# Kernel tuning notes

Measured on AMD Instinct MI355X. Metric: run time of the kernel, lower is better.

Reference implementation:

```python
import jax, jax.numpy as jnp
import numpy as np
from jax import lax

GAMMA = 1.0  # init gamma


def setup_inputs() -> dict:
    key = jax.random.key(0)
    k = jax.random.split(key, 6)
    B, T1, T2, D, WD = 64, 320, 320, 768, 32
    x = jax.random.normal(k[0], (B, T1, D), jnp.float32)
    y = jax.random.normal(k[1], (B, T2, D), jnp.float32)
    # nn.Linear(input_dim, warp_dim): weight [WD, D], bias [WD]
    W = jax.random.normal(k[2], (WD, D), jnp.float32) / np.sqrt(D).astype(np.float32)
    b = 0.01 * jax.random.normal(k[3], (WD,), jnp.float32)
    warp_scale = 1.0 + 0.1 * jax.random.normal(k[4], (WD,), jnp.float32)
    warp_shift = 0.1 * jax.random.normal(k[5], (WD,), jnp.float32)
    return {"x": x, "y": y, "W": W, "b": b, "warp_scale": warp_scale, "warp_shift": warp_shift}


def _soft_dtw_path(xw, yw, gamma):
    # Faithful banded soft-DTW DP: cells outside the band stay 0 and ARE read
    # by in-band neighbors, exactly as the torch loop does.
    B, T1, _ = xw.shape
    T2 = yw.shape[1]
    bw = max(T1, T2) // 4 + 1
    # squared euclidean distances [B,T1,T2] (expanded form to avoid B*T1*T2*D blow-up)
    x2 = jnp.sum(xw * xw, -1)[:, :, None]
    y2 = jnp.sum(yw * yw, -1)[:, None, :]
    dist = x2 + y2 - 2.0 * jnp.einsum('bid,bjd->bij', xw, yw)
    NEG = jnp.float32(-1e30)  # disables a candidate inside logsumexp
    t2s = jnp.arange(T2)

    def outer(prev_row, xs):  # prev_row: path[t1-1, :] of shape [B,T2]
        t1, drow = xs  # drow: dist[:, t1, :] -> [B,T2]
        diag_prev = jnp.concatenate([jnp.zeros((B, 1), drow.dtype), prev_row[:, :-1]], axis=1)

        def inner(left, ins):  # left: path[t1, t2-1] -> [B]
            t2, d, up, diag = ins
            z = jnp.stack([
                jnp.where((t1 > 0) & (t2 > 0), -diag / gamma, NEG),
                jnp.where(t1 > 0, -up / gamma, NEG),
                jnp.where(t2 > 0, -left / gamma, NEG),
            ], axis=0)  # [3,B]
            softmin = -gamma * jax.nn.logsumexp(z, axis=0)
            val = d + jnp.where((t1 > 0) | (t2 > 0), softmin, 0.0)
            in_band = (t2 >= t1 - bw) & (t2 <= t1 + bw - 1)
            val = jnp.where(in_band, val, 0.0)
            return val, val

        _, row = lax.scan(inner, jnp.zeros((B,), drow.dtype),
                          (t2s, drow.T, prev_row.T, diag_prev.T))
        row = row.T  # [B,T2]
        return row, row

    _, path = lax.scan(outer, jnp.zeros((B, T2), dist.dtype),
                       (jnp.arange(T1), jnp.transpose(dist, (1, 0, 2))))
    path = jnp.transpose(path, (1, 0, 2))  # [B,T1,T2]
    return jax.nn.softmax(-path / gamma, axis=-1)


def reference(x, y, W, b, warp_scale, warp_shift):
    xw = (x @ W.T + b) * warp_scale + warp_shift
    yw = (y @ W.T + b) * warp_scale + warp_shift
    path = _soft_dtw_path(xw, yw, GAMMA)  # [B,T1,T2] softmax probs
    pn = path / (jnp.sum(path, axis=1, keepdims=True) + 1e-10)
    aligned = jnp.einsum('bts,btd->bsd', pn, x)  # bmm(path^T, x) -> [B,T2,D]
    return aligned, path
```

## Files before the change

kernel.cpp:

```cpp
#include <hip/hip_runtime.h>

#define NB 64
#define T 320
#define D 768
#define WD 32
#define NSTEP 639
#define NBLK 80
#define BSTRIDE (NBLK * 1024)
#define BIG 1e30f
#define LOG2E 1.44269504088896340736f
#define LN2 0.69314718055994530942f

__device__ __forceinline__ float dpp_ror1(float v) {
  return __int_as_float(__builtin_amdgcn_update_dpp(
      0, __float_as_int(v), 0x13C, 0xF, 0xF, true));
}
__device__ __forceinline__ float dpp_rol1(float v) {
  return __int_as_float(__builtin_amdgcn_update_dpp(
      0, __float_as_int(v), 0x134, 0xF, 0xF, true));
}

__global__ __launch_bounds__(256) void prep_kernel(
    const float* __restrict__ W, const float* __restrict__ bias,
    const float* __restrict__ wscale, const float* __restrict__ wshift,
    float* __restrict__ WeT, float* __restrict__ beff) {
  int i = blockIdx.x * 256 + threadIdx.x;
  int c = i >> 5, k = i & 31;
  WeT[i] = W[k * D + c] * wscale[k];
  if (i < WD) beff[i] = bias[i] * wscale[i] + wshift[i];
}

__global__ __launch_bounds__(256) void proj_kernel(
    const float* __restrict__ x, const float* __restrict__ y,
    const float* __restrict__ WeT, const float* __restrict__ beff,
    float* __restrict__ xw, float* __restrict__ yw) {
  __shared__ float lds[8448];
  int tid = threadIdx.x;
  int w = tid >> 6, l = tid & 63;
  int rbase = blockIdx.x * 64;
  float acc[32];
#pragma unroll
  for (int k = 0; k < 32; ++k) acc[k] = 0.f;
#pragma clang loop unroll(disable)
  for (int ch = 0; ch < 6; ++ch) {
    __syncthreads();
#pragma unroll
    for (int p = 0; p < 8; ++p) {
      int idx = p * 256 + tid;
      int row = idx >> 5;
      int c4 = idx & 31;
      int r = rbase + row;
      const float* src = (r < NB * T) ? x + (size_t)r * D
                                      : y + (size_t)(r - NB * T) * D;
      float4 v = *(const float4*)(src + ch * 128 + c4 * 4);
      lds[row * 129 + c4 * 4 + 0] = v.x;
      lds[row * 129 + c4 * 4 + 1] = v.y;
      lds[row * 129 + c4 * 4 + 2] = v.z;
      lds[row * 129 + c4 * 4 + 3] = v.w;
    }
    __syncthreads();
    int woff = __builtin_amdgcn_readfirstlane((ch * 128 + w * 32) * 32);
    const float* wp = WeT + woff;
#pragma unroll
    for (int cc = 0; cc < 32; ++cc) {
      float xv = lds[l * 129 + w * 32 + cc];
#pragma unroll
      for (int k = 0; k < 32; ++k)
        acc[k] = fmaf(wp[cc * 32 + k], xv, acc[k]);
    }
  }
  __syncthreads();
#pragma unroll
  for (int k = 0; k < 32; ++k) lds[w * 2112 + l * 33 + k] = acc[k];
  __syncthreads();
  int idx = tid * 8;
  int row = idx >> 5;
  int k0 = idx & 31;
  float o[8];
#pragma unroll
  for (int e = 0; e < 8; ++e)
    o[e] = lds[0 * 2112 + row * 33 + k0 + e] + lds[1 * 2112 + row * 33 + k0 + e] +
           lds[2 * 2112 + row * 33 + k0 + e] + lds[3 * 2112 + row * 33 + k0 + e] +
           beff[k0 + e];
  int rr = rbase + row;
  float* dst = (rr < NB * T) ? xw + (size_t)rr * WD + k0
                             : yw + (size_t)(rr - NB * T) * WD + k0;
  float4 o0 = {o[0], o[1], o[2], o[3]}, o1 = {o[4], o[5], o[6], o[7]};
  *(float4*)dst = o0;
  *(float4*)(dst + 4) = o1;
}

__global__ __launch_bounds__(256) void dist_kernel(
    const float* __restrict__ xw, const float* __restrict__ yw,
    float* __restrict__ dc) {
  int b = blockIdx.y;
  int i = blockIdx.x * 256 + threadIdx.x;
  int dblk = i >> 10;
  int a = (i >> 3) & 127;
  int k = i & 7;
  if (a >= 81) return;
  int d = dblk * 8 + k;
  if (d >= NSTEP) return;
  int par = (d + 1) & 1;
  int base = (d + 81 - par) >> 1;
  int t1 = base - a;
  int t2 = d - t1;
  if ((unsigned)t1 >= (unsigned)T || (unsigned)t2 >= (unsigned)T) return;
  const float4* xr = (const float4*)(xw + ((size_t)b * T + t1) * WD);
  const float4* yr = (const float4*)(yw + ((size_t)b * T + t2) * WD);
  float s = 0.f;
#pragma unroll
  for (int q = 0; q < 8; ++q) {
    float4 xv = xr[q], yv = yr[q];
    float d0 = xv.x - yv.x, d1 = xv.y - yv.y, d2 = xv.z - yv.z, d3 = xv.w - yv.w;
    s = fmaf(d0, d0, s); s = fmaf(d1, d1, s); s = fmaf(d2, d2, s); s = fmaf(d3, d3, s);
  }
  dc[(size_t)b * BSTRIDE + i] = s * LOG2E;
}

#define FSTEP(DP_, DS_, PAR, DVAL)                                             \
  {                                                                            \
    const int d_ = (DVAL);                                                     \
    const int base_ = (d_ + 81 - (PAR)) >> 1;                                  \
    float shP, shS;                                                            \
    if (PAR) { shP = dpp_rol1((l == 0) ? v0b : v0); shS = dpp_rol1(v0b); }     \
    else     { shP = dpp_ror1(v1); shS = dpp_ror1((l == 63) ? v1 : v1b); }     \
    int t1 = base_ - l, t2 = d_ - t1;                                          \
    {                                                                          \
      bool valid = ((unsigned)t1 < (unsigned)T) && ((unsigned)t2 < (unsigned)T); \
      float up, left, diag;                                                    \
      if (PAR) { left = v0; up = shP; diag = v1; }                             \
      else     { up = v1; left = (l == 0) ? 0.f : shP; diag = v0; }            \
      float cu = (t1 > 0) ? up : BIG;                                          \
      float cl = (t2 > 0) ? left : BIG;                                        \
      float cd = (t1 > 0 && t2 > 0) ? diag : BIG;                              \
      float mn = fminf(fminf(cu, cl), cd);                                     \
      float mx = fmaxf(fmaxf(cu, cl), cd);                                     \
      float md = fmaxf(fminf(cu, cl), fminf(fmaxf(cu, cl), cd));               \
      float ss = 1.f + __builtin_amdgcn_exp2f(mn - md) +                       \
                 __builtin_amdgcn_exp2f(mn - mx);                              \
      float val = (DP_) + mn - __builtin_amdgcn_logf(ss);                      \
      if ((DVAL) == 0) val = (DP_);                                            \
      if (valid) {                                                             \
        if (PAR) v1 = val; else v0 = val;                                      \
        outb[t1 * T + t2] = val * LN2;                                         \
      }                                                                        \
    }                                                                          \
    {                                                                          \
      int t1b = t1 - 64, t2b = t2 + 64;                                        \
      bool valid = (l < 17) && ((unsigned)t1b < (unsigned)T) &&                \
                   ((unsigned)t2b < (unsigned)T);                              \
      float up, left, diag;                                                    \
      if (PAR) { left = v0b; up = (l == 16) ? 0.f : shS; diag = v1b; }         \
      else     { up = v1b; left = shS; diag = v0b; }                           \
      float cu = (t1b > 0) ? up : BIG;                                         \
      float cl = (t2b > 0) ? left : BIG;                                       \
      float cd = (t1b > 0 && t2b > 0) ? diag : BIG;                            \
      float mn = fminf(fminf(cu, cl), cd);                                     \
      float mx = fmaxf(fmaxf(cu, cl), cd);                                     \
      float md = fmaxf(fminf(cu, cl), fminf(fmaxf(cu, cl), cd));               \
      float ss = 1.f + __builtin_amdgcn_exp2f(mn - md) +                       \
                 __builtin_amdgcn_exp2f(mn - mx);                              \
      float val = (DS_) + mn - __builtin_amdgcn_logf(ss);                      \
      if (valid) {                                                             \
        if (PAR) v1b = val; else v0b = val;                                    \
        outb[t1b * T + t2b] = val * LN2;                                       \
      }                                                                        \
    }                                                                          \
  }

#define SSTEP(DP_, DS_, PAR, IOFF)                                             \
  {                                                                            \
    float shP, shS;                                                            \
    if (PAR) { shP = dpp_rol1((l == 0) ? v0b : v0); shS = dpp_rol1(v0b); }     \
    else     { shP = dpp_ror1(v1); shS = dpp_ror1((l == 63) ? v1 : v1b); }     \
    {                                                                          \
      float up, left, diag;                                                    \
      if (PAR) { left = v0; up = shP; diag = v1; }                             \
      else     { up = v1; left = (l == 0) ? 0.f : shP; diag = v0; }            \
      float mn = fminf(fminf(up, left), diag);                                 \
      float mx = fmaxf(fmaxf(up, left), diag);                                 \
      float md = fmaxf(fminf(up, left), fminf(fmaxf(up, left), diag));         \
      float ss = 1.f + __builtin_amdgcn_exp2f(mn - md) +                       \
                 __builtin_amdgcn_exp2f(mn - mx);                              \
      float val = (DP_) + mn - __builtin_amdgcn_logf(ss);                      \
      if (PAR) v1 = val; else v0 = val;                                        \
      outb[io + (IOFF)] = val * LN2;                                           \
    }                                                                          \
    {                                                                          \
      float up, left, diag;                                                    \
      if (PAR) { left = v0b; up = (l == 16) ? 0.f : shS; diag = v1b; }         \
      else     { up = v1b; left = shS; diag = v0b; }                           \
      float mn = fminf(fminf(up, left), diag);                                 \
      float mx = fmaxf(fmaxf(up, left), diag);                                 \
      float md = fmaxf(fminf(up, left), fminf(fmaxf(up, left), diag));         \
      float ss = 1.f + __builtin_amdgcn_exp2f(mn - md) +                       \
                 __builtin_amdgcn_exp2f(mn - mx);                              \
      float val = (DS_) + mn - __builtin_amdgcn_logf(ss);                      \
      if (PAR) v1b = val; else v0b = val;                                      \
      if (l < 17) outb[ioS + (IOFF)] = val * LN2;                              \
    }                                                                          \
  }

#define LOADBLK(R0, R1, S0v, S1v, DBLK)                                        \
  {                                                                            \
    const float4* q_ = (const float4*)(dcb + (DBLK) * 1024 + l * 8);           \
    R0 = q_[0]; R1 = q_[1];                                                    \
    const float4* q2_ = (const float4*)(dcb + (DBLK) * 1024 + (64 + l) * 8);   \
    S0v = q2_[0]; S1v = q2_[1];                                                \
  }

#define BLK8_F(P0, P1, S0v, S1v, DB)                                           \
  FSTEP(P0.x, S0v.x, 1, (DB) + 0) FSTEP(P0.y, S0v.y, 0, (DB) + 1)              \
  FSTEP(P0.z, S0v.z, 1, (DB) + 2) FSTEP(P0.w, S0v.w, 0, (DB) + 3)              \
  FSTEP(P1.x, S1v.x, 1, (DB) + 4) FSTEP(P1.y, S1v.y, 0, (DB) + 5)              \
  FSTEP(P1.z, S1v.z, 1, (DB) + 6) FSTEP(P1.w, S1v.w, 0, (DB) + 7)

#define BLK8_S(P0, P1, S0v, S1v)                                               \
  SSTEP(P0.x, S0v.x, 1, 0)   SSTEP(P0.y, S0v.y, 0, 320)                        \
  SSTEP(P0.z, S0v.z, 1, 321) SSTEP(P0.w, S0v.w, 0, 641)                        \
  io += 642; ioS += 642;                                                       \
  SSTEP(P1.x, S1v.x, 1, 0)   SSTEP(P1.y, S1v.y, 0, 320)                        \
  SSTEP(P1.z, S1v.z, 1, 321) SSTEP(P1.w, S1v.w, 0, 641)                        \
  io += 642; ioS += 642;

__global__ __launch_bounds__(64) void dtw_kernel(
    const float* __restrict__ dc, float* __restrict__ path) {
  int b = blockIdx.x;
  int l = threadIdx.x;
  const float* dcb = dc + (size_t)b * BSTRIDE;
  float* outb = path + (size_t)b * T * T;
  float v0 = 0.f, v1 = 0.f, v0b = 0.f, v1b = 0.f;
  float4 aP0, aP1, aS0, aS1, bP0, bP1, bS0, bS1;
  int io = 0, ioS = 0;

  if (l == 40) {
    float d00 = dcb[320];
    v1 = d00;
    outb[0] = d00 * LN2;
  }
  LOADBLK(aP0, aP1, aS0, aS1, 0)
#pragma clang loop unroll(disable)
  for (int it = 0; it < 6; ++it) {
    int dbase = it * 16;
    int blk = it * 2;
    LOADBLK(bP0, bP1, bS0, bS1, blk + 1)
    BLK8_F(aP0, aP1, aS0, aS1, dbase)
    LOADBLK(aP0, aP1, aS0, aS1, blk + 2)
    BLK8_F(bP0, bP1, bS0, bS1, dbase + 8)
  }
  io = 28168 - 319 * l;
  ioS = io - 20416;
#pragma clang loop unroll(disable)
  for (int it = 0; it < 27; ++it) {
    int blk = 12 + it * 2;
    LOADBLK(bP0, bP1, bS0, bS1, blk + 1)
    BLK8_S(aP0, aP1, aS0, aS1)
    LOADBLK(aP0, aP1, aS0, aS1, blk + 2)
    BLK8_S(bP0, bP1, bS0, bS1)
  }
#pragma clang loop unroll(disable)
  for (int it = 0; it < 6; ++it) {
    int dbase = 528 + it * 16;
    int blk = 66 + it * 2;
    LOADBLK(bP0, bP1, bS0, bS1, blk + 1)
    BLK8_F(aP0, aP1, aS0, aS1, dbase)
    LOADBLK(aP0, aP1, aS0, aS1, blk + 2)
    BLK8_F(bP0, bP1, bS0, bS1, dbase + 8)
  }
  LOADBLK(bP0, bP1, bS0, bS1, 79)
  BLK8_F(aP0, aP1, aS0, aS1, 624)
  FSTEP(bP0.x, bS0.x, 1, 632) FSTEP(bP0.y, bS0.y, 0, 633)
  FSTEP(bP0.z, bS0.z, 1, 634) FSTEP(bP0.w, bS0.w, 0, 635)
  FSTEP(bP1.x, bS1.x, 1, 636) FSTEP(bP1.y, bS1.y, 0, 637)
  FSTEP(bP1.z, bS1.z, 1, 638)
}

__global__ __launch_bounds__(T) void softmax_kernel(float* __restrict__ path,
                                                    float* __restrict__ cvec) {
  __shared__ float sm1[5], sm2[5];
  int row = blockIdx.x;
  int t1 = row % T;
  int j = threadIdx.x;
  float* p = path + (size_t)row * T;
  bool in = (j >= t1 - 81) && (j <= t1 + 80);
  float v = in ? p[j] : 0.f;
  float m = v;
#pragma unroll
  for (int off = 32; off >= 1; off >>= 1) m = fminf(m, __shfl_xor(m, off, 64));
  int w = j >> 6;
  if ((j & 63) == 0) sm1[w] = m;
  __syncthreads();
  m = fminf(fminf(fminf(sm1[0], sm1[1]), fminf(sm1[2], sm1[3])), sm1[4]);
  float e = __expf(m - v);
  float s = e;
#pragma unroll
  for (int off = 32; off >= 1; off >>= 1) s += __shfl_xor(s, off, 64);
  if ((j & 63) == 0) sm2[w] = s;
  __syncthreads();
  s = sm2[0] + sm2[1] + sm2[2] + sm2[3] + sm2[4];
  p[j] = e / s;
  if (j == 0) cvec[row] = __expf(m - 0.f) / s;
}

__global__ __launch_bounds__(256) void gk_kernel(
    const float* __restrict__ x, const float* __restrict__ cvec,
    float* __restrict__ g) {
  int b = blockIdx.y;
  int d0 = blockIdx.x * 256 + threadIdx.x;
  const float* xb = x + (size_t)b * T * D + d0;
  const float* cb = cvec + b * T;
  float s = 0.f;
  for (int t = 0; t < T; ++t) s = fmaf(cb[t], xb[(size_t)t * D], s);
  g[b * D + d0] = s;
}

__global__ __launch_bounds__(T) void colsum_kernel(
    const float* __restrict__ path, float* __restrict__ scale) {
  int b = blockIdx.x;
  int j = threadIdx.x;
  const float* p = path + (size_t)b * T * T;
  float s = 0.f;
  for (int t = 0; t < T; ++t) s += p[(size_t)t * T + j];
  scale[b * T + j] = 1.f / (s + 1e-10f);
}

#define TSB 64
#define TDB 256
#define TKB 16
__global__ __launch_bounds__(256) void bmm_kernel(
    const float* __restrict__ path, const float* __restrict__ x,
    const float* __restrict__ cvec, const float* __restrict__ g,
    const float* __restrict__ scale, float* __restrict__ out) {
  __shared__ __align__(16) float Pl[TKB][TSB];
  __shared__ __align__(16) float Xl[TKB][TDB];
  int b = blockIdx.z;
  int s0 = blockIdx.y * TSB;
  int d0 = blockIdx.x * TDB;
  int tid = threadIdx.x;
  int ts = tid & 7, td = tid >> 3;
  const float* pb = path + (size_t)b * T * T;
  const float* xb = x + (size_t)b * T * D;
  const float* cb = cvec + b * T;
  float acc[8][8];
  {
    const float* gb = g + b * D + d0 + td * 8;
    float4 g0 = *(const float4*)gb;
    float4 g1 = *(const float4*)(gb + 4);
    float gv[8] = {g0.x, g0.y, g0.z, g0.w, g1.x, g1.y, g1.z, g1.w};
#pragma unroll
    for (int i = 0; i < 8; ++i)
#pragma unroll
      for (int jj = 0; jj < 8; ++jj) acc[i][jj] = gv[jj];
  }
  int t_lo = s0 - 80; if (t_lo < 0) t_lo = 0; t_lo &= ~15;
  int t_hi = (s0 + 160) & ~15; if (t_hi > T) t_hi = T;
  for (int t0 = t_lo; t0 < t_hi; t0 += TKB) {
    __syncthreads();
    {
      int tr = tid >> 4, sc = (tid & 15) * 4;
      float4 p4 = *(const float4*)&pb[(size_t)(t0 + tr) * T + s0 + sc];
      float cv = cb[t0 + tr];
      p4.x -= cv; p4.y -= cv; p4.z -= cv; p4.w -= cv;
      *(float4*)&Pl[tr][sc] = p4;
    }
    {
      int tr = tid >> 4, c0 = (tid & 15) * 4;
#pragma unroll
      for (int q = 0; q < 4; ++q)
        *(float4*)&Xl[tr][c0 + q * 64] =
            *(const float4*)&xb[(size_t)(t0 + tr) * D + d0 + c0 + q * 64];
    }
    __syncthreads();
#pragma unroll
    for (int t = 0; t < TKB; ++t) {
      float4 pa = *(const float4*)&Pl[t][ts * 8];
      float4 pc = *(const float4*)&Pl[t][ts * 8 + 4];
      float4 xa = *(const float4*)&Xl[t][td * 8];
      float4 xc = *(const float4*)&Xl[t][td * 8 + 4];
      float pv[8] = {pa.x, pa.y, pa.z, pa.w, pc.x, pc.y, pc.z, pc.w};
      float xv[8] = {xa.x, xa.y, xa.z, xa.w, xc.x, xc.y, xc.z, xc.w};
#pragma unroll
      for (int i = 0; i < 8; ++i)
#pragma unroll
        for (int jj = 0; jj < 8; ++jj)
          acc[i][jj] = fmaf(pv[i], xv[jj], acc[i][jj]);
    }
  }
#pragma unroll
  for (int i = 0; i < 8; ++i) {
    int s = s0 + ts * 8 + i;
    float sc = scale[b * T + s];
    float* op = out + ((size_t)b * T + s) * D + d0 + td * 8;
    float4 o0, o1;
    o0.x = acc[i][0] * sc; o0.y = acc[i][1] * sc; o0.z = acc[i][2] * sc; o0.w = acc[i][3] * sc;
    o1.x = acc[i][4] * sc; o1.y = acc[i][5] * sc; o1.z = acc[i][6] * sc; o1.w = acc[i][7] * sc;
    *(float4*)op = o0;
    *(float4*)(op + 4) = o1;
  }
}

extern "C" void kernel_launch(void* const* d_in, const int* in_sizes, int n_in,
                              void* d_out, int out_size, void* d_ws, size_t ws_size,
                              hipStream_t stream) {
  const float* x = (const float*)d_in[0];
  const float* y = (const float*)d_in[1];
  const float* W = (const float*)d_in[2];
  const float* bias = (const float*)d_in[3];
  const float* wscale = (const float*)d_in[4];
  const float* wshift = (const float*)d_in[5];
  float* outp = (float*)d_out;
  float* aligned = outp;
  float* path = outp + (size_t)NB * T * D;
  float* distc = aligned;
  float* ws = (float*)d_ws;
  float* xw = ws;
  float* yw = xw + (size_t)NB * T * WD;
  float* scale = yw + (size_t)NB * T * WD;
  float* WeT = scale + (size_t)NB * T;
  float* beff = WeT + (size_t)WD * D;
  float* cvec = beff + WD;
  float* g = cvec + (size_t)NB * T;

  prep_kernel<<<dim3((WD * D) / 256), 256, 0, stream>>>(W, bias, wscale, wshift, WeT, beff);
  proj_kernel<<<dim3((2 * NB * T) / 64), 256, 0, stream>>>(x, y, WeT, beff, xw, yw);
  dist_kernel<<<dim3(BSTRIDE / 256, NB), 256, 0, stream>>>(xw, yw, distc);
  dtw_kernel<<<dim3(NB), 64, 0, stream>>>(distc, path);
  softmax_kernel<<<dim3(NB * T), T, 0, stream>>>(path, cvec);
  gk_kernel<<<dim3(D / 256, NB), 256, 0, stream>>>(x, cvec, g);
  colsum_kernel<<<dim3(NB), T, 0, stream>>>(path, scale);
  bmm_kernel<<<dim3(D / TDB, T / TSB, NB), 256, 0, stream>>>(path, x, cvec, g, scale, aligned);
}
```

Before: 374.5 us.

## Double-buffer bmm tiles, remap blocks for XCD locality, band-limit colsum

The bmm kernel now prefetches the next path/x tile into registers while computing on the current shared-memory buffer, and writes it into a second buffer, so there is one barrier per chunk instead of two. A 1D grid is remapped so consecutive blocks spread across XCDs while related tiles share L2. The colsum kernel uses more blocks and reads only the band region of each column, adding back the per-row constant cvec for out-of-band entries. The band-limited colsum depends on softmax values outside the band equaling cvec, and double buffering doubles shared memory per block.

Result: slower. 410.7 us (+9.7%).

```diff
diff --git a/kernel.cpp b/kernel.cpp
--- a/kernel.cpp
+++ b/kernel.cpp
@@ -315,14 +315,36 @@
   g[b * D + d0] = s;
 }
 
-__global__ __launch_bounds__(T) void colsum_kernel(
-    const float* __restrict__ path, float* __restrict__ scale) {
-  int b = blockIdx.x;
-  int j = threadIdx.x;
-  const float* p = path + (size_t)b * T * T;
+__global__ __launch_bounds__(256) void colsum_kernel(
+    const float* __restrict__ path, const float* __restrict__ cvec,
+    float* __restrict__ scale) {
+  __shared__ float red[4][64];
+  __shared__ float cbred[4];
+  int b = blockIdx.y;
+  int tid = threadIdx.x;
+  int l = tid & 63, tq = tid >> 6;
+  int j = blockIdx.x * 64 + l;
+  const float* cb = cvec + b * T;
+  float c = cb[tid];
+  if (tid < 64) c += cb[256 + tid];
+#pragma unroll
+  for (int off = 32; off >= 1; off >>= 1) c += __shfl_xor(c, off, 64);
+  if (l == 0) cbred[tq] = c;
   float s = 0.f;
-  for (int t = 0; t < T; ++t) s += p[(size_t)t * T + j];
-  scale[b * T + j] = 1.f / (s + 1e-10f);
+  int t0 = j - 80 + tq * 41;
+  const float* p = path + (size_t)b * T * T + j;
+#pragma unroll 4
+  for (int i = 0; i < 41; ++i) {
+    int t = t0 + i;
+    if ((unsigned)t < (unsigned)T) s += p[(size_t)t * T] - cb[t];
+  }
+  red[tq][l] = s;
+  __syncthreads();
+  if (tq == 0) {
+    float cs = red[0][l] + red[1][l] + red[2][l] + red[3][l] +
+               (cbred[0] + cbred[1] + cbred[2] + cbred[3]);
+    scale[b * T + j] = 1.f / (cs + 1e-10f);
+  }
 }
 
 #define TSB 64
@@ -332,11 +354,14 @@
     const float* __restrict__ path, const float* __restrict__ x,
     const float* __restrict__ cvec, const float* __restrict__ g,
     const float* __restrict__ scale, float* __restrict__ out) {
-  __shared__ __align__(16) float Pl[TKB][TSB];
-  __shared__ __align__(16) float Xl[TKB][TDB];
-  int b = blockIdx.z;
-  int s0 = blockIdx.y * TSB;
-  int d0 = blockIdx.x * TDB;
+  __shared__ __align__(16) float Pl[2][TKB][TSB];
+  __shared__ __align__(16) float Xl[2][TKB][TDB];
+  int bid = blockIdx.x;
+  int wgid = (bid & 7) * 120 + (bid >> 3);
+  int b = wgid / 15;
+  int r = wgid - b * 15;
+  int s0 = (r / 3) * TSB;
+  int d0 = (r % 3) * TDB;
   int tid = threadIdx.x;
   int ts = tid & 7, td = tid >> 3;
   const float* pb = path + (size_t)b * T * T;
@@ -355,29 +380,44 @@
   }
   int t_lo = s0 - 80; if (t_lo < 0) t_lo = 0; t_lo &= ~15;
   int t_hi = (s0 + 160) & ~15; if (t_hi > T) t_hi = T;
-  for (int t0 = t_lo; t0 < t_hi; t0 += TKB) {
-    __syncthreads();
-    {
-      int tr = tid >> 4, sc = (tid & 15) * 4;
-      float4 p4 = *(const float4*)&pb[(size_t)(t0 + tr) * T + s0 + sc];
-      float cv = cb[t0 + tr];
-      p4.x -= cv; p4.y -= cv; p4.z -= cv; p4.w -= cv;
-      *(float4*)&Pl[tr][sc] = p4;
-    }
-    {
-      int tr = tid >> 4, c0 = (tid & 15) * 4;
-#pragma unroll
-      for (int q = 0; q < 4; ++q)
-        *(float4*)&Xl[tr][c0 + q * 64] =
-            *(const float4*)&xb[(size_t)(t0 + tr) * D + d0 + c0 + q * 64];
-    }
-    __syncthreads();
+  int nch = (t_hi - t_lo) >> 4;
+  int str = tid >> 4;
+  int psc = (tid & 15) * 4;
+  float4 pr, xr0, xr1, xr2, xr3;
+  float cvr;
+#define BMM_LOAD(T0)                                                        \
+  {                                                                         \
+    pr = *(const float4*)&pb[(size_t)((T0) + str) * T + s0 + psc];          \
+    cvr = cb[(T0) + str];                                                   \
+    const float* xrow = &xb[(size_t)((T0) + str) * D + d0 + psc];           \
+    xr0 = *(const float4*)(xrow);                                           \
+    xr1 = *(const float4*)(xrow + 64);                                      \
+    xr2 = *(const float4*)(xrow + 128);                                     \
+    xr3 = *(const float4*)(xrow + 192);                                     \
+  }
+#define BMM_WRITE(BUF)                                                      \
+  {                                                                         \
+    float4 pw = pr;                                                         \
+    pw.x -= cvr; pw.y -= cvr; pw.z -= cvr; pw.w -= cvr;                     \
+    *(float4*)&Pl[BUF][str][psc] = pw;                                      \
+    *(float4*)&Xl[BUF][str][psc] = xr0;                                     \
+    *(float4*)&Xl[BUF][str][psc + 64] = xr1;                                \
+    *(float4*)&Xl[BUF][str][psc + 128] = xr2;                               \
+    *(float4*)&Xl[BUF][str][psc + 192] = xr3;                               \
+  }
+  BMM_LOAD(t_lo)
+  BMM_WRITE(0)
+  __syncthreads();
+  int cur = 0;
+#pragma clang loop unroll(disable)
+  for (int ch = 0; ch < nch; ++ch) {
+    if (ch + 1 < nch) { BMM_LOAD(t_lo + (ch + 1) * TKB) }
 #pragma unroll
     for (int t = 0; t < TKB; ++t) {
-      float4 pa = *(const float4*)&Pl[t][ts * 8];
-      float4 pc = *(const float4*)&Pl[t][ts * 8 + 4];
-      float4 xa = *(const float4*)&Xl[t][td * 8];
-      float4 xc = *(const float4*)&Xl[t][td * 8 + 4];
+      float4 pa = *(const float4*)&Pl[cur][t][ts * 8];
+      float4 pc = *(const float4*)&Pl[cur][t][ts * 8 + 4];
+      float4 xa = *(const float4*)&Xl[cur][t][td * 8];
+      float4 xc = *(const float4*)&Xl[cur][t][td * 8 + 4];
       float pv[8] = {pa.x, pa.y, pa.z, pa.w, pc.x, pc.y, pc.z, pc.w};
       float xv[8] = {xa.x, xa.y, xa.z, xa.w, xc.x, xc.y, xc.z, xc.w};
 #pragma unroll
@@ -385,6 +425,11 @@
 #pragma unroll
         for (int jj = 0; jj < 8; ++jj)
           acc[i][jj] = fmaf(pv[i], xv[jj], acc[i][jj]);
+    }
+    if (ch + 1 < nch) {
+      BMM_WRITE(cur ^ 1)
+      __syncthreads();
+      cur ^= 1;
     }
   }
 #pragma unroll
@@ -428,6 +473,6 @@
   dtw_kernel<<<dim3(NB), 64, 0, stream>>>(distc, path);
   softmax_kernel<<<dim3(NB * T), T, 0, stream>>>(path, cvec);
   gk_kernel<<<dim3(D / 256, NB), 256, 0, stream>>>(x, cvec, g);
-  colsum_kernel<<<dim3(NB), T, 0, stream>>>(path, scale);
-  bmm_kernel<<<dim3(D / TDB, T / TSB, NB), 256, 0, stream>>>(path, x, cvec, g, scale, aligned);
-}
+  colsum_kernel<<<dim3(T / 64, NB), 256, 0, stream>>>(path, cvec, scale);
+  bmm_kernel<<<dim3((D / TDB) * (T / TSB) * NB), 256, 0, stream>>>(path, x, cvec, g, scale, aligned);
+}
```

## Band-limit column sums via cvec baseline and remap bmm blocks for XCD locality

Applied to the files above, without the earlier changes.

The column-sum kernel now reads only a band of about 164 rows per column and adds the constant out-of-band contribution as the total of cvec, computed with a wave shuffle reduction. It also spreads the work over more blocks (5 per batch, 4 waves each) instead of one block of 320 threads per batch. The bmm launch becomes a 1D grid whose block index is remapped so that consecutive blocks going to the same XCD share a batch, aiming for better L2 reuse. This relies on out-of-band path values equalling cvec exactly, the same assumption the bmm kernel already makes.

New measurement: 378.8 us. About the same (+1.2%).

```diff
diff --git a/kernel.cpp b/kernel.cpp
--- a/kernel.cpp
+++ b/kernel.cpp
@@ -315,14 +315,36 @@
   g[b * D + d0] = s;
 }
 
-__global__ __launch_bounds__(T) void colsum_kernel(
-    const float* __restrict__ path, float* __restrict__ scale) {
-  int b = blockIdx.x;
-  int j = threadIdx.x;
-  const float* p = path + (size_t)b * T * T;
+__global__ __launch_bounds__(256) void colsum_kernel(
+    const float* __restrict__ path, const float* __restrict__ cvec,
+    float* __restrict__ scale) {
+  __shared__ float red[4][64];
+  __shared__ float cbred[4];
+  int b = blockIdx.y;
+  int tid = threadIdx.x;
+  int l = tid & 63, tq = tid >> 6;
+  int j = blockIdx.x * 64 + l;
+  const float* cb = cvec + b * T;
+  float c = cb[tid];
+  if (tid < 64) c += cb[256 + tid];
+#pragma unroll
+  for (int off = 32; off >= 1; off >>= 1) c += __shfl_xor(c, off, 64);
+  if (l == 0) cbred[tq] = c;
   float s = 0.f;
-  for (int t = 0; t < T; ++t) s += p[(size_t)t * T + j];
-  scale[b * T + j] = 1.f / (s + 1e-10f);
+  int t0 = j - 80 + tq * 41;
+  const float* p = path + (size_t)b * T * T + j;
+#pragma unroll 4
+  for (int i = 0; i < 41; ++i) {
+    int t = t0 + i;
+    if ((unsigned)t < (unsigned)T) s += p[(size_t)t * T] - cb[t];
+  }
+  red[tq][l] = s;
+  __syncthreads();
+  if (tq == 0) {
+    float cs = red[0][l] + red[1][l] + red[2][l] + red[3][l] +
+               (cbred[0] + cbred[1] + cbred[2] + cbred[3]);
+    scale[b * T + j] = 1.f / (cs + 1e-10f);
+  }
 }
 
 #define TSB 64
@@ -334,9 +356,12 @@
     const float* __restrict__ scale, float* __restrict__ out) {
   __shared__ __align__(16) float Pl[TKB][TSB];
   __shared__ __align__(16) float Xl[TKB][TDB];
-  int b = blockIdx.z;
-  int s0 = blockIdx.y * TSB;
-  int d0 = blockIdx.x * TDB;
+  int bid = blockIdx.x;
+  int wgid = (bid & 7) * 120 + (bid >> 3);
+  int b = wgid / 15;
+  int r = wgid - b * 15;
+  int s0 = (r / 3) * TSB;
+  int d0 = (r % 3) * TDB;
   int tid = threadIdx.x;
   int ts = tid & 7, td = tid >> 3;
   const float* pb = path + (size_t)b * T * T;
@@ -428,6 +453,6 @@
   dtw_kernel<<<dim3(NB), 64, 0, stream>>>(distc, path);
   softmax_kernel<<<dim3(NB * T), T, 0, stream>>>(path, cvec);
   gk_kernel<<<dim3(D / 256, NB), 256, 0, stream>>>(x, cvec, g);
-  colsum_kernel<<<dim3(NB), T, 0, stream>>>(path, scale);
-  bmm_kernel<<<dim3(D / TDB, T / TSB, NB), 256, 0, stream>>>(path, x, cvec, g, scale, aligned);
-}
+  colsum_kernel<<<dim3(T / 64, NB), 256, 0, stream>>>(path, cvec, scale);
+  bmm_kernel<<<dim3((D / TDB) * (T / TSB) * NB), 256, 0, stream>>>(path, x, cvec, g, scale, aligned);
+}
```
